# Performance work log

Hardware: AMD Instinct MI355X
Metric: run time of the kernel (lower is better)

The kernel has to match this reference:

```python
import jax, jax.numpy as jnp
import numpy as np

GAMMA = 1.0

def setup_inputs() -> dict:
    key = jax.random.key(0)
    kx, ky = jax.random.split(key)
    x = jax.random.normal(kx, (8192, 256), dtype=jnp.float32)
    y = jax.random.normal(ky, (8192, 256), dtype=jnp.float32)
    return {"x": x, "y": y}

def reference(x, y):
    # RBF kernel K[i,j] = exp(-gamma * ||x_i - y_j||^2)
    # materializing the O(N*M*D) broadcast difference tensor.
    x2 = jnp.sum(x * x, axis=-1)            # [N]
    y2 = jnp.sum(y * y, axis=-1)            # [M]
    xy = jnp.einsum('nd,md->nm', x, y)      # [N, M] GEMM
    dist2 = x2[:, None] + y2[None, :] - 2.0 * xy
    dist2 = jnp.maximum(dist2, 0.0)         # guard tiny negative round-off
    return jnp.exp(-GAMMA * dist2)
```

## Files before the change

### kernel.cpp

```cpp
#include <hip/hip_runtime.h>


#define M_DIM 8192
#define K_DIM 256
#define BM 128
#define BN 128
#define BK 64

typedef __attribute__((ext_vector_type(8))) short short8;
typedef __attribute__((ext_vector_type(4))) float float4v;

__device__ inline unsigned short f2bf(float f) {
    union { float f; unsigned int u; } a; a.f = f;
    unsigned int u = a.u;
    unsigned int r = u + 0x7fffu + ((u >> 16) & 1u);
    return (unsigned short)(r >> 16);
}

__global__ __launch_bounds__(256) void prep_kernel(
        const float* __restrict__ x, const float* __restrict__ y,
        unsigned short* __restrict__ xb, unsigned short* __restrict__ yb,
        float* __restrict__ x2, float* __restrict__ y2) {
    int row  = blockIdx.x * 4 + (threadIdx.x >> 6);
    int lane = threadIdx.x & 63;

    const float* src; unsigned short* dst; float* nrm; int r;
    if (row < M_DIM) { src = x; dst = xb; nrm = x2; r = row; }
    else             { src = y; dst = yb; nrm = y2; r = row - M_DIM; }

    const float4* s4 = (const float4*)(src + (size_t)r * K_DIM);
    float4 v = s4[lane];
    float ss = v.x * v.x + v.y * v.y + v.z * v.z + v.w * v.w;

    ushort4 p;
    p.x = f2bf(v.x); p.y = f2bf(v.y); p.z = f2bf(v.z); p.w = f2bf(v.w);
    ((ushort4*)(dst + (size_t)r * K_DIM))[lane] = p;

    #pragma unroll
    for (int o = 32; o > 0; o >>= 1) ss += __shfl_down(ss, o);
    if (lane == 0) nrm[r] = ss;
}

__global__ __launch_bounds__(256, 3) void rbf_gemm(
        const unsigned short* __restrict__ xb, const unsigned short* __restrict__ yb,
        const float* __restrict__ x2, const float* __restrict__ y2,
        float* __restrict__ out) {
    __shared__ __align__(16) unsigned short As[BM * BK];
    __shared__ __align__(16) unsigned short Bs[BN * BK];

    const int tid  = threadIdx.x;
    const int wid  = tid >> 6;
    const int lane = tid & 63;
    const int wm   = wid >> 1;
    const int wn   = wid & 1;

    const int bid = blockIdx.x;
    const int xcd = bid & 7;
    const int lin = bid >> 3;
    const int ty  = (xcd << 3) + (lin >> 6);
    const int tx  = lin & 63;
    const int m0  = ty * BM;
    const int n0  = tx * BN;

    float4v acc[4][4] = {};

    const int lrow8 = lane >> 3;
    const int lchk  = lane & 7;

    for (int kt = 0; kt < K_DIM; kt += BK) {
        #pragma unroll
        for (int i = 0; i < 4; ++i) {
            int rbase = i * 32 + wid * 8;
            const unsigned short* ga = xb
                + (size_t)(m0 + rbase + lrow8) * K_DIM + kt + lchk * 8;
            __builtin_amdgcn_global_load_lds(
                (__attribute__((address_space(1))) void*)ga,
                (__attribute__((address_space(3))) void*)&As[rbase * BK],
                16, 0, 0);
        }
        #pragma unroll
        for (int i = 0; i < 4; ++i) {
            int rbase = i * 32 + wid * 8;
            const unsigned short* gb = yb
                + (size_t)(n0 + rbase + lrow8) * K_DIM + kt + lchk * 8;
            __builtin_amdgcn_global_load_lds(
                (__attribute__((address_space(1))) void*)gb,
                (__attribute__((address_space(3))) void*)&Bs[rbase * BK],
                16, 0, 0);
        }
        __syncthreads();

        #pragma unroll
        for (int ks = 0; ks < 2; ++ks) {
            const int colk = ks * 32 + (lane >> 4) * 8;
            short8 af[4], bfr[4];
            #pragma unroll
            for (int mt = 0; mt < 4; ++mt)
                af[mt] = *(const short8*)&As[(wm * 64 + mt * 16 + (lane & 15)) * BK + colk];
            #pragma unroll
            for (int nt = 0; nt < 4; ++nt)
                bfr[nt] = *(const short8*)&Bs[(wn * 64 + nt * 16 + (lane & 15)) * BK + colk];
            #pragma unroll
            for (int mt = 0; mt < 4; ++mt)
                #pragma unroll
                for (int nt = 0; nt < 4; ++nt)
                    acc[mt][nt] = __builtin_amdgcn_mfma_f32_16x16x32_bf16(
                        af[mt], bfr[nt], acc[mt][nt], 0, 0, 0);
        }
        __syncthreads();
    }

    const int q = lane >> 4;
    const int c = lane & 15;
    #pragma unroll
    for (int mt = 0; mt < 4; ++mt) {
        const int rowb = m0 + wm * 64 + mt * 16 + q * 4;
        float x2v[4];
        #pragma unroll
        for (int v = 0; v < 4; ++v) x2v[v] = x2[rowb + v];
        #pragma unroll
        for (int nt = 0; nt < 4; ++nt) {
            const int col = n0 + wn * 64 + nt * 16 + c;
            const float y2v = y2[col];
            #pragma unroll
            for (int v = 0; v < 4; ++v) {
                float d = x2v[v] + y2v - 2.0f * acc[mt][nt][v];
                d = fmaxf(d, 0.0f);
                out[(size_t)(rowb + v) * M_DIM + col] = __expf(-d);
            }
        }
    }
}

__global__ void rbf_naive(const float* __restrict__ x, const float* __restrict__ y,
                          float* __restrict__ out) {
    __shared__ float xs[16][17];
    __shared__ float ys[16][17];
    const int tx = threadIdx.x, ty = threadIdx.y;
    const int row = blockIdx.y * 16 + ty;
    const int col = blockIdx.x * 16 + tx;
    float acc = 0.0f;
    for (int k0 = 0; k0 < K_DIM; k0 += 16) {
        xs[ty][tx] = x[(size_t)row * K_DIM + k0 + tx];
        ys[ty][tx] = y[(size_t)(blockIdx.x * 16 + ty) * K_DIM + k0 + tx];
        __syncthreads();
        #pragma unroll
        for (int kk = 0; kk < 16; ++kk) {
            float d = xs[ty][kk] - ys[tx][kk];
            acc += d * d;
        }
        __syncthreads();
    }
    out[(size_t)row * M_DIM + col] = __expf(-acc);
}

extern "C" void kernel_launch(void* const* d_in, const int* in_sizes, int n_in,
                              void* d_out, int out_size, void* d_ws, size_t ws_size,
                              hipStream_t stream) {
    const float* x = (const float*)d_in[0];
    const float* y = (const float*)d_in[1];
    float* out = (float*)d_out;

    const size_t need = (size_t)2 * M_DIM * K_DIM * sizeof(unsigned short)
                      + (size_t)2 * M_DIM * sizeof(float);
    if (ws_size >= need) {
        unsigned short* xb = (unsigned short*)d_ws;
        unsigned short* yb = xb + (size_t)M_DIM * K_DIM;
        float* x2 = (float*)(yb + (size_t)M_DIM * K_DIM);
        float* y2 = x2 + M_DIM;

        prep_kernel<<<dim3((2 * M_DIM) / 4), dim3(256), 0, stream>>>(x, y, xb, yb, x2, y2);
        rbf_gemm<<<dim3((M_DIM / BM) * (M_DIM / BN)), dim3(256), 0, stream>>>(xb, yb, x2, y2, out);
    } else {
        rbf_naive<<<dim3(M_DIM / 16, M_DIM / 16), dim3(16, 16), 0, stream>>>(x, y, out);
    }
}
```

Measured before the change: 296.2 us.

## Switch GEMM to FP8 MFMA with full-K LDS tile and XOR swizzle

```diff
diff --git a/kernel.cpp b/kernel.cpp
--- a/kernel.cpp
+++ b/kernel.cpp
@@ -5,26 +5,18 @@
 #define K_DIM 256
 #define BM 128
 #define BN 128
-#define BK 64
 
-typedef __attribute__((ext_vector_type(8))) short short8;
+typedef long frag8;
 typedef __attribute__((ext_vector_type(4))) float float4v;
-
-__device__ inline unsigned short f2bf(float f) {
-    union { float f; unsigned int u; } a; a.f = f;
-    unsigned int u = a.u;
-    unsigned int r = u + 0x7fffu + ((u >> 16) & 1u);
-    return (unsigned short)(r >> 16);
-}
 
 __global__ __launch_bounds__(256) void prep_kernel(
         const float* __restrict__ x, const float* __restrict__ y,
-        unsigned short* __restrict__ xb, unsigned short* __restrict__ yb,
+        unsigned char* __restrict__ xb, unsigned char* __restrict__ yb,
         float* __restrict__ x2, float* __restrict__ y2) {
     int row  = blockIdx.x * 4 + (threadIdx.x >> 6);
     int lane = threadIdx.x & 63;
 
-    const float* src; unsigned short* dst; float* nrm; int r;
+    const float* src; unsigned char* dst; float* nrm; int r;
     if (row < M_DIM) { src = x; dst = xb; nrm = x2; r = row; }
     else             { src = y; dst = yb; nrm = y2; r = row - M_DIM; }
 
@@ -32,21 +24,25 @@
     float4 v = s4[lane];
     float ss = v.x * v.x + v.y * v.y + v.z * v.z + v.w * v.w;
 
-    ushort4 p;
-    p.x = f2bf(v.x); p.y = f2bf(v.y); p.z = f2bf(v.z); p.w = f2bf(v.w);
-    ((ushort4*)(dst + (size_t)r * K_DIM))[lane] = p;
+    int packed = __builtin_amdgcn_cvt_pk_fp8_f32(v.x, v.y, 0, false);
+    packed     = __builtin_amdgcn_cvt_pk_fp8_f32(v.z, v.w, packed, true);
+
+    int u  = lane >> 2;
+    int su = u ^ (r & 15);
+    *(unsigned int*)(dst + (size_t)r * 256 + su * 16 + (lane & 3) * 4) =
+        (unsigned int)packed;
 
     #pragma unroll
     for (int o = 32; o > 0; o >>= 1) ss += __shfl_down(ss, o);
     if (lane == 0) nrm[r] = ss;
 }
 
-__global__ __launch_bounds__(256, 3) void rbf_gemm(
-        const unsigned short* __restrict__ xb, const unsigned short* __restrict__ yb,
+__global__ __launch_bounds__(256, 2) void rbf_gemm(
+        const unsigned char* __restrict__ xb, const unsigned char* __restrict__ yb,
         const float* __restrict__ x2, const float* __restrict__ y2,
         float* __restrict__ out) {
-    __shared__ __align__(16) unsigned short As[BM * BK];
-    __shared__ __align__(16) unsigned short Bs[BN * BK];
+    __shared__ __align__(16) unsigned char As[BM * 256];
+    __shared__ __align__(16) unsigned char Bs[BN * 256];
 
     const int tid  = threadIdx.x;
     const int wid  = tid >> 6;
@@ -62,52 +58,47 @@
     const int m0  = ty * BM;
     const int n0  = tx * BN;
 
+    #pragma unroll
+    for (int i = 0; i < 8; ++i) {
+        const int c = wid * 8 + i;
+        __builtin_amdgcn_global_load_lds(
+            (__attribute__((address_space(1))) void*)
+                (xb + (size_t)(m0 + c * 4) * 256 + lane * 16),
+            (__attribute__((address_space(3))) void*)&As[c * 1024],
+            16, 0, 0);
+    }
+    #pragma unroll
+    for (int i = 0; i < 8; ++i) {
+        const int c = wid * 8 + i;
+        __builtin_amdgcn_global_load_lds(
+            (__attribute__((address_space(1))) void*)
+                (yb + (size_t)(n0 + c * 4) * 256 + lane * 16),
+            (__attribute__((address_space(3))) void*)&Bs[c * 1024],
+            16, 0, 0);
+    }
+    __syncthreads();
+
+    const int fr = lane & 15;
+    const int g  = lane >> 4;
+
     float4v acc[4][4] = {};
 
-    const int lrow8 = lane >> 3;
-    const int lchk  = lane & 7;
-
-    for (int kt = 0; kt < K_DIM; kt += BK) {
+    #pragma unroll
+    for (int ks = 0; ks < 8; ++ks) {
+        const int off = (((2 * ks + (g >> 1)) ^ fr) << 4) + (g & 1) * 8;
+        frag8 af[4], bf[4];
         #pragma unroll
-        for (int i = 0; i < 4; ++i) {
-            int rbase = i * 32 + wid * 8;
-            const unsigned short* ga = xb
-                + (size_t)(m0 + rbase + lrow8) * K_DIM + kt + lchk * 8;
-            __builtin_amdgcn_global_load_lds(
-                (__attribute__((address_space(1))) void*)ga,
-                (__attribute__((address_space(3))) void*)&As[rbase * BK],
-                16, 0, 0);
-        }
+        for (int mt = 0; mt < 4; ++mt)
+            af[mt] = *(const frag8*)&As[(wm * 64 + mt * 16 + fr) * 256 + off];
         #pragma unroll
-        for (int i = 0; i < 4; ++i) {
-            int rbase = i * 32 + wid * 8;
-            const unsigned short* gb = yb
-                + (size_t)(n0 + rbase + lrow8) * K_DIM + kt + lchk * 8;
-            __builtin_amdgcn_global_load_lds(
-                (__attribute__((address_space(1))) void*)gb,
-                (__attribute__((address_space(3))) void*)&Bs[rbase * BK],
-                16, 0, 0);
-        }
-        __syncthreads();
-
+        for (int nt = 0; nt < 4; ++nt)
+            bf[nt] = *(const frag8*)&Bs[(wn * 64 + nt * 16 + fr) * 256 + off];
         #pragma unroll
-        for (int ks = 0; ks < 2; ++ks) {
-            const int colk = ks * 32 + (lane >> 4) * 8;
-            short8 af[4], bfr[4];
-            #pragma unroll
-            for (int mt = 0; mt < 4; ++mt)
-                af[mt] = *(const short8*)&As[(wm * 64 + mt * 16 + (lane & 15)) * BK + colk];
+        for (int mt = 0; mt < 4; ++mt)
             #pragma unroll
             for (int nt = 0; nt < 4; ++nt)
-                bfr[nt] = *(const short8*)&Bs[(wn * 64 + nt * 16 + (lane & 15)) * BK + colk];
-            #pragma unroll
-            for (int mt = 0; mt < 4; ++mt)
-                #pragma unroll
-                for (int nt = 0; nt < 4; ++nt)
-                    acc[mt][nt] = __builtin_amdgcn_mfma_f32_16x16x32_bf16(
-                        af[mt], bfr[nt], acc[mt][nt], 0, 0, 0);
-        }
-        __syncthreads();
+                acc[mt][nt] = __builtin_amdgcn_mfma_f32_16x16x32_fp8_fp8(
+                    af[mt], bf[nt], acc[mt][nt], 0, 0, 0);
     }
 
     const int q = lane >> 4;
@@ -161,12 +152,12 @@
     const float* y = (const float*)d_in[1];
     float* out = (float*)d_out;
 
-    const size_t need = (size_t)2 * M_DIM * K_DIM * sizeof(unsigned short)
+    const size_t need = (size_t)2 * M_DIM * 256
                       + (size_t)2 * M_DIM * sizeof(float);
     if (ws_size >= need) {
-        unsigned short* xb = (unsigned short*)d_ws;
-        unsigned short* yb = xb + (size_t)M_DIM * K_DIM;
-        float* x2 = (float*)(yb + (size_t)M_DIM * K_DIM);
+        unsigned char* xb = (unsigned char*)d_ws;
+        unsigned char* yb = xb + (size_t)M_DIM * 256;
+        float* x2 = (float*)(yb + (size_t)M_DIM * 256);
         float* y2 = x2 + M_DIM;
 
         prep_kernel<<<dim3((2 * M_DIM) / 4), dim3(256), 0, stream>>>(x, y, xb, yb, x2, y2);
```

Result: faster. 284.0 us (-4.1%).
